# Performance work log

Measured on AMD Instinct MI355X. Metric: run time of the kernel, lower is better.

Reference implementation:

```python
import jax, jax.numpy as jnp
import numpy as np

# Dims: B=8 episodes, N=5 ways, K=5 shots -> BNK=200; L=128 tokens; D=O=1024; R=50 dep relations.
BNK, L, D, O, R = 200, 128, 1024, 1024, 50
M = BNK * L  # flattened token count


def setup_inputs() -> dict:
    key = jax.random.key(0)
    ks = jax.random.split(key, 12)
    rep = jax.random.normal(ks[0], (BNK, L, D), dtype=jnp.float32)
    # edge list: (source sentence in [0,BNK), source token in [0,L))
    arc_sent = jax.random.randint(ks[1], (M, 1), 0, BNK, dtype=jnp.int32)
    arc_tok = jax.random.randint(ks[2], (M, 1), 0, L, dtype=jnp.int32)
    adj_arc_in = jnp.concatenate([arc_sent, arc_tok], axis=1)
    adj_lab_in = jax.random.randint(ks[3], (M,), 0, R, dtype=jnp.int32)
    adj_mask_in = (jax.random.uniform(ks[4], (M, 1)) < 0.9).astype(jnp.float32)
    adj_mask_loop = jnp.ones((M, 1), dtype=jnp.float32)
    mask = (jax.random.uniform(ks[5], (BNK, L)) < 0.9).astype(jnp.float32)
    xav = (2.0 / (D + O)) ** 0.5  # xavier_normal std
    W_in = jax.random.normal(ks[6], (D, O), dtype=jnp.float32) * xav
    b_in = jnp.zeros((R, O), dtype=jnp.float32)
    W_gate_in = jax.random.uniform(ks[7], (D, 1), dtype=jnp.float32)
    b_gate_in = jnp.ones((R, 1), dtype=jnp.float32)
    W_self = jax.random.normal(ks[8], (D, O), dtype=jnp.float32) * xav
    W_gate_self = jax.random.uniform(ks[9], (D, 1), dtype=jnp.float32)
    return {
        "rep": rep, "adj_arc_in": adj_arc_in, "adj_lab_in": adj_lab_in,
        "adj_mask_in": adj_mask_in, "adj_mask_loop": adj_mask_loop, "mask": mask,
        "W_in": W_in, "b_in": b_in, "W_gate_in": W_gate_in, "b_gate_in": b_gate_in,
        "W_self": W_self, "W_gate_self": W_gate_self,
    }


def reference(rep, adj_arc_in, adj_lab_in, adj_mask_in, adj_mask_loop, mask,
              W_in, b_in, W_gate_in, b_gate_in, W_self, W_gate_self):
    bnk, l, d = rep.shape
    o = W_in.shape[1]
    rep_ = rep.reshape(bnk * l, d)                          # (M, D)
    idx = adj_arc_in[:, 0] * l + adj_arc_in[:, 1]           # (M,) flat gather index
    # in-arc potentials: gather projected source token + relation bias
    in_ = (rep_ @ W_in)[idx] + b_in[adj_lab_in]             # (M, O)
    in_gate = (rep_ @ W_gate_in)[idx] + b_gate_in[adj_lab_in]  # (M, 1)
    # self-loop potentials
    same_ = rep_ @ W_self                                   # (M, O)
    same_gate = rep_ @ W_gate_self                          # (M, 1)
    pot = jnp.stack([in_, same_], axis=1)                   # (M, deg=2, O)
    gates = jnp.concatenate([in_gate, same_gate], axis=1)   # (M, 2)
    mask_soft = jnp.concatenate([adj_mask_in, adj_mask_loop], axis=1)  # (M, 2)
    # faithful to original: potentials * mask_soft * (sigmoid(gate) * mask_soft)
    w = mask_soft * (jax.nn.sigmoid(gates) * mask_soft)     # (M, 2)
    out = jax.nn.relu(jnp.einsum('mdo,md->mo', pot, w))     # (M, O)
    return out.reshape(bnk, l, o) * mask[:, :, None]
```

## Files before the change

### kernel.cpp

```cpp
#include <hip/hip_runtime.h>

constexpr int BNKv = 200, Lv = 128, Dv = 1024, Ov = 1024;
constexpr int Mv = BNKv * Lv;
constexpr int KA = 1024;
constexpr int NB = 2048;
constexpr int NT = KA / 64;

using u16 = unsigned short;
typedef __bf16 bf16x8 __attribute__((ext_vector_type(8)));
typedef float f32x4 __attribute__((ext_vector_type(4)));

__device__ __forceinline__ u16 f2bf(float x) {
    unsigned int u = __float_as_uint(x);
    u += 0x7fffu + ((u >> 16) & 1u);
    return (u16)(u >> 16);
}

#define MEMBAR() asm volatile("" ::: "memory")
__device__ __forceinline__ void sbar() {
    MEMBAR(); __builtin_amdgcn_s_barrier(); MEMBAR();
}


__global__ __launch_bounds__(256) void convert_rep(
    const float* __restrict__ rep,
    const float* __restrict__ wg_in,
    const float* __restrict__ wg_self,
    u16* __restrict__ Ap,
    float* __restrict__ gout_in,
    float* __restrict__ gout_self)
{
    const int m = blockIdx.x;
    const int t = threadIdx.x;
    const float4 x  = *(const float4*)(rep + (size_t)m * Dv + t * 4);
    const float4 wi = *(const float4*)(wg_in + t * 4);
    const float4 wsf= *(const float4*)(wg_self + t * 4);

    ushort4 hv = make_ushort4(f2bf(x.x), f2bf(x.y), f2bf(x.z), f2bf(x.w));
    const int cs = (t * 4) ^ ((m & 7) << 3);
    *(ushort4*)(Ap + (size_t)m * KA + cs) = hv;

    float gi = x.x * wi.x + x.y * wi.y + x.z * wi.z + x.w * wi.w;
    float gs = x.x * wsf.x + x.y * wsf.y + x.z * wsf.z + x.w * wsf.w;
#pragma unroll
    for (int off = 32; off > 0; off >>= 1) {
        gi += __shfl_down(gi, off);
        gs += __shfl_down(gs, off);
    }
    __shared__ float ri[4], rs[4];
    if ((t & 63) == 0) { ri[t >> 6] = gi; rs[t >> 6] = gs; }
    __syncthreads();
    if (t == 0) {
        gout_in[m]   = ri[0] + ri[1] + ri[2] + ri[3];
        gout_self[m] = rs[0] + rs[1] + rs[2] + rs[3];
    }
}

__global__ __launch_bounds__(256) void convert_w(
    const float* __restrict__ W0, const float* __restrict__ W1,
    u16* __restrict__ Bt)
{
    const float* W = blockIdx.z ? W1 : W0;
    u16* B = Bt + (size_t)blockIdx.z * 1024 * KA;
    const int kt = blockIdx.x, nt = blockIdx.y;
    __shared__ float tile[64][65];
    const int tid = threadIdx.x;
    const int c = tid & 63, r4 = tid >> 6;
#pragma unroll 4
    for (int it = 0; it < 16; ++it) {
        int kl = it * 4 + r4;
        tile[kl][c] = W[(size_t)(kt * 64 + kl) * Ov + nt * 64 + c];
    }
    __syncthreads();
#pragma unroll 4
    for (int it = 0; it < 16; ++it) {
        int nl = it * 4 + r4;
        const int n = nt * 64 + nl;
        const int kx = kt * 64 + (c ^ ((n & 7) << 3));
        B[(size_t)n * KA + kx] = f2bf(tile[c][nl]);
    }
}

__global__ __launch_bounds__(512) void gemm8p(
    const u16* __restrict__ A, const u16* __restrict__ Bt,
    float* __restrict__ P)
{
    __shared__ u16 As[2][2][128][64];
    __shared__ u16 Bs[2][2][128][64];

    const int tid = threadIdx.x;
    const int l = tid & 63;
    const int w = tid >> 6;
    const int wr = w >> 2;
    const int wc = w & 3;
    const int hc = wc >> 1;
    const int mt = blockIdx.x >> 3;
    const int nt = blockIdx.x & 7;
    const int gm0 = mt * 256, gn0 = nt * 256;
    const int lrow = l & 15;
    const int lk = (l >> 4) * 8;
    const int swz = (lrow & 7) << 3;
    const int c0 = lk ^ swz, c1 = (32 + lk) ^ swz;
    const int srow = w * 8 + (l >> 3);
    const int scol = (l & 7) * 8;

    auto stageA = [&](int kt, int h, int b) {
        const int kb = kt * 64;
#pragma unroll
        for (int r = 0; r < 2; ++r) {
            const u16* g = A + (size_t)(gm0 + h * 128 + r * 64 + srow) * KA + kb + scol;
            __builtin_amdgcn_global_load_lds(
                (const __attribute__((address_space(1))) void*)g,
                (__attribute__((address_space(3))) void*)(&As[b][h][r * 64 + w * 8][0]),
                16, 0, 0);
        }
    };
    auto stageB = [&](int kt, int h, int b) {
        const int kb = kt * 64;
#pragma unroll
        for (int r = 0; r < 2; ++r) {
            const u16* g = Bt + (size_t)(gn0 + h * 128 + r * 64 + srow) * KA + kb + scol;
            __builtin_amdgcn_global_load_lds(
                (const __attribute__((address_space(1))) void*)g,
                (__attribute__((address_space(3))) void*)(&Bs[b][h][r * 64 + w * 8][0]),
                16, 0, 0);
        }
    };

    f32x4 acc[8][4];
#pragma unroll
    for (int i = 0; i < 8; ++i)
#pragma unroll
        for (int j = 0; j < 4; ++j) acc[i][j] = (f32x4){0.f, 0.f, 0.f, 0.f};

    stageA(0, 0, 0); stageA(0, 1, 0); stageB(0, 0, 0); stageB(0, 1, 0);
    stageA(1, 0, 1); stageA(1, 1, 1); stageB(1, 0, 1); stageB(1, 1, 1);
    asm volatile("s_waitcnt vmcnt(8)" ::: "memory");
    sbar();

    bf16x8 aR[4][2];
    bf16x8 bQ[2][2][2];

    for (int kt = 0; kt < NT; ++kt) {
        const int cur = kt & 1;
        const bool st2 = (kt + 2 < NT);

#pragma unroll
        for (int mi = 0; mi < 4; ++mi) {
            aR[mi][0] = *(const bf16x8*)&As[cur][wr][mi * 16 + lrow][c0];
            aR[mi][1] = *(const bf16x8*)&As[cur][wr][mi * 16 + lrow][c1];
        }
#pragma unroll
        for (int nj = 0; nj < 2; ++nj) {
            bQ[0][nj][0] = *(const bf16x8*)&Bs[cur][hc][(wc & 1) * 64 + nj * 16 + lrow][c0];
            bQ[0][nj][1] = *(const bf16x8*)&Bs[cur][hc][(wc & 1) * 64 + nj * 16 + lrow][c1];
        }
        __builtin_amdgcn_s_setprio(1);
#pragma unroll
        for (int mi = 0; mi < 4; ++mi)
#pragma unroll
            for (int nj = 0; nj < 2; ++nj)
#pragma unroll
                for (int ks = 0; ks < 2; ++ks)
                    acc[mi][nj] = __builtin_amdgcn_mfma_f32_16x16x32_bf16(
                        aR[mi][ks], bQ[0][nj][ks], acc[mi][nj], 0, 0, 0);
        __builtin_amdgcn_s_setprio(0);
        sbar();

#pragma unroll
        for (int nj = 0; nj < 2; ++nj) {
            bQ[1][nj][0] = *(const bf16x8*)&Bs[cur][hc][(wc & 1) * 64 + 32 + nj * 16 + lrow][c0];
            bQ[1][nj][1] = *(const bf16x8*)&Bs[cur][hc][(wc & 1) * 64 + 32 + nj * 16 + lrow][c1];
        }
        __builtin_amdgcn_s_setprio(1);
#pragma unroll
        for (int mi = 0; mi < 4; ++mi)
#pragma unroll
            for (int nj = 0; nj < 2; ++nj)
#pragma unroll
                for (int ks = 0; ks < 2; ++ks)
                    acc[mi][2 + nj] = __builtin_amdgcn_mfma_f32_16x16x32_bf16(
                        aR[mi][ks], bQ[1][nj][ks], acc[mi][2 + nj], 0, 0, 0);
        __builtin_amdgcn_s_setprio(0);
        sbar();

#pragma unroll
        for (int mi = 0; mi < 4; ++mi) {
            aR[mi][0] = *(const bf16x8*)&As[cur][wr][64 + mi * 16 + lrow][c0];
            aR[mi][1] = *(const bf16x8*)&As[cur][wr][64 + mi * 16 + lrow][c1];
        }
        if (st2) { stageB(kt + 2, 0, cur); stageB(kt + 2, 1, cur); }
        __builtin_amdgcn_s_setprio(1);
#pragma unroll
        for (int mi = 0; mi < 4; ++mi)
#pragma unroll
            for (int nj = 0; nj < 2; ++nj)
#pragma unroll
                for (int ks = 0; ks < 2; ++ks)
                    acc[4 + mi][nj] = __builtin_amdgcn_mfma_f32_16x16x32_bf16(
                        aR[mi][ks], bQ[0][nj][ks], acc[4 + mi][nj], 0, 0, 0);
        __builtin_amdgcn_s_setprio(0);
        sbar();

        if (st2) { stageA(kt + 2, 0, cur); stageA(kt + 2, 1, cur); }
        __builtin_amdgcn_s_setprio(1);
#pragma unroll
        for (int mi = 0; mi < 4; ++mi)
#pragma unroll
            for (int nj = 0; nj < 2; ++nj)
#pragma unroll
                for (int ks = 0; ks < 2; ++ks)
                    acc[4 + mi][2 + nj] = __builtin_amdgcn_mfma_f32_16x16x32_bf16(
                        aR[mi][ks], bQ[1][nj][ks], acc[4 + mi][2 + nj], 0, 0, 0);
        __builtin_amdgcn_s_setprio(0);
        if (st2) { asm volatile("s_waitcnt vmcnt(8)" ::: "memory"); }
        else     { asm volatile("s_waitcnt vmcnt(0)" ::: "memory"); }
        sbar();
    }

    const int orow = (l >> 4) * 4, ocol = l & 15;
#pragma unroll
    for (int mi = 0; mi < 8; ++mi)
#pragma unroll
        for (int nj = 0; nj < 4; ++nj) {
            const int col = gn0 + wc * 64 + nj * 16 + ocol;
#pragma unroll
            for (int r = 0; r < 4; ++r) {
                const int row = gm0 + wr * 128 + mi * 16 + orow + r;
                P[(size_t)row * NB + col] = acc[mi][nj][r];
            }
        }
}

__global__ __launch_bounds__(256) void epilogue(
    const float* __restrict__ P,
    const float* __restrict__ g_in, const float* __restrict__ g_self,
    const int* __restrict__ arc, const int* __restrict__ lab,
    const float* __restrict__ am_in, const float* __restrict__ am_loop,
    const float* __restrict__ maskBL,
    const float* __restrict__ b_in, const float* __restrict__ b_gate_in,
    float* __restrict__ out)
{
    const int m = blockIdx.x;
    const int t = threadIdx.x;
    __shared__ float sw0, sw1;
    __shared__ int sgidx, slab;
    if (t == 0) {
        const int gidx = arc[2 * m] * Lv + arc[2 * m + 1];
        const int lb = lab[m];
        const float am = am_in[m], lp = am_loop[m], mk = maskBL[m];
        const float gi = g_in[gidx] + b_gate_in[lb];
        const float gs = g_self[m];
        sw0 = am * am * (1.f / (1.f + expf(-gi))) * mk;
        sw1 = lp * lp * (1.f / (1.f + expf(-gs))) * mk;
        sgidx = gidx;
        slab = lb;
    }
    __syncthreads();
    const float w0 = sw0, w1 = sw1;
    const int c = t * 4;
    const float4 pin = *(const float4*)(P + (size_t)sgidx * NB + c);
    const float4 bi  = *(const float4*)(b_in + (size_t)slab * Ov + c);
    const float4 ps  = *(const float4*)(P + (size_t)m * NB + 1024 + c);
    float4 o;
    o.x = fmaxf(w0 * (pin.x + bi.x) + w1 * ps.x, 0.f);
    o.y = fmaxf(w0 * (pin.y + bi.y) + w1 * ps.y, 0.f);
    o.z = fmaxf(w0 * (pin.z + bi.z) + w1 * ps.z, 0.f);
    o.w = fmaxf(w0 * (pin.w + bi.w) + w1 * ps.w, 0.f);
    *(float4*)(out + (size_t)m * Ov + c) = o;
}

constexpr size_t SZ_A  = (size_t)Mv * KA * 2;
constexpr size_t SZ_B  = (size_t)NB * KA * 2;
constexpr size_t OFF_A  = 0;
constexpr size_t OFF_B  = OFF_A + SZ_A;
constexpr size_t OFF_GI = OFF_B + SZ_B;
constexpr size_t OFF_GS = OFF_GI + (size_t)Mv * 4;
constexpr size_t OFF_P  = OFF_GS + (size_t)Mv * 4;

extern "C" void kernel_launch(void* const* d_in, const int* in_sizes, int n_in,
                              void* d_out, int out_size, void* d_ws, size_t ws_size,
                              hipStream_t stream) {
    const float* rep       = (const float*)d_in[0];
    const int*   arc       = (const int*)d_in[1];
    const int*   lab       = (const int*)d_in[2];
    const float* am_in     = (const float*)d_in[3];
    const float* am_loop   = (const float*)d_in[4];
    const float* maskBL    = (const float*)d_in[5];
    const float* W_in      = (const float*)d_in[6];
    const float* b_in      = (const float*)d_in[7];
    const float* W_gate_in = (const float*)d_in[8];
    const float* b_gate_in = (const float*)d_in[9];
    const float* W_self    = (const float*)d_in[10];
    const float* W_gate_self = (const float*)d_in[11];
    float* out = (float*)d_out;
    char* ws = (char*)d_ws;

    u16*   Ap  = (u16*)(ws + OFF_A);
    u16*   Bt  = (u16*)(ws + OFF_B);
    float* gIn = (float*)(ws + OFF_GI);
    float* gSf = (float*)(ws + OFF_GS);
    float* P   = (float*)(ws + OFF_P);

    convert_rep<<<Mv, 256, 0, stream>>>(rep, W_gate_in, W_gate_self, Ap, gIn, gSf);
    convert_w<<<dim3(16, 16, 2), 256, 0, stream>>>(W_in, W_self, Bt);

    const int gemm_grid = (Mv / 256) * (NB / 256);
    gemm8p<<<gemm_grid, 512, 0, stream>>>(Ap, Bt, P);

    epilogue<<<Mv, 256, 0, stream>>>(P, gIn, gSf, arc, lab, am_in, am_loop,
                                     maskBL, b_in, b_gate_in, out);
}
```

Baseline: 396.1 us.

## Split GEMM into two launches and fuse gather epilogue into self-loop GEMM

The single 2048-wide GEMM is split into two launches. The first computes rep@W_in into a 1024-wide buffer. The second computes rep@W_self and applies the gate, gather, bias, ReLU and mask epilogue directly from the accumulators, which drops the separate epilogue kernel and the write and read-back of the self-loop half of P. convert_rep is also reworked so each wave handles one row, with four rows per block, removing the shared-memory reduction and barrier. The cost is two serialized GEMM launches, and the fused epilogue does scattered per-row gathers from Pin with scalar loads.

```diff
diff --git a/kernel.cpp b/kernel.cpp
--- a/kernel.cpp
+++ b/kernel.cpp
@@ -3,7 +3,6 @@
 constexpr int BNKv = 200, Lv = 128, Dv = 1024, Ov = 1024;
 constexpr int Mv = BNKv * Lv;
 constexpr int KA = 1024;
-constexpr int NB = 2048;
 constexpr int NT = KA / 64;
 
 using u16 = unsigned short;
@@ -30,30 +29,31 @@
     float* __restrict__ gout_in,
     float* __restrict__ gout_self)
 {
-    const int m = blockIdx.x;
-    const int t = threadIdx.x;
-    const float4 x  = *(const float4*)(rep + (size_t)m * Dv + t * 4);
-    const float4 wi = *(const float4*)(wg_in + t * 4);
-    const float4 wsf= *(const float4*)(wg_self + t * 4);
-
-    ushort4 hv = make_ushort4(f2bf(x.x), f2bf(x.y), f2bf(x.z), f2bf(x.w));
-    const int cs = (t * 4) ^ ((m & 7) << 3);
-    *(ushort4*)(Ap + (size_t)m * KA + cs) = hv;
-
-    float gi = x.x * wi.x + x.y * wi.y + x.z * wi.z + x.w * wi.w;
-    float gs = x.x * wsf.x + x.y * wsf.y + x.z * wsf.z + x.w * wsf.w;
+    const int row = blockIdx.x * 4 + (threadIdx.x >> 6);
+    const int l = threadIdx.x & 63;
+    const float4* rp  = (const float4*)(rep + (size_t)row * Dv);
+    const float4* wip = (const float4*)wg_in;
+    const float4* wsp = (const float4*)wg_self;
+    u16* ap = Ap + (size_t)row * KA;
+    const int sw = (row & 7) << 3;
+    float gi = 0.f, gs = 0.f;
+#pragma unroll
+    for (int j = 0; j < 4; ++j) {
+        const int c4 = j * 64 + l;
+        const float4 x  = rp[c4];
+        const float4 wi = wip[c4];
+        const float4 wf = wsp[c4];
+        ushort4 hv = make_ushort4(f2bf(x.x), f2bf(x.y), f2bf(x.z), f2bf(x.w));
+        *(ushort4*)(ap + ((c4 * 4) ^ sw)) = hv;
+        gi += x.x * wi.x + x.y * wi.y + x.z * wi.z + x.w * wi.w;
+        gs += x.x * wf.x + x.y * wf.y + x.z * wf.z + x.w * wf.w;
+    }
 #pragma unroll
     for (int off = 32; off > 0; off >>= 1) {
         gi += __shfl_down(gi, off);
         gs += __shfl_down(gs, off);
     }
-    __shared__ float ri[4], rs[4];
-    if ((t & 63) == 0) { ri[t >> 6] = gi; rs[t >> 6] = gs; }
-    __syncthreads();
-    if (t == 0) {
-        gout_in[m]   = ri[0] + ri[1] + ri[2] + ri[3];
-        gout_self[m] = rs[0] + rs[1] + rs[2] + rs[3];
-    }
+    if (l == 0) { gout_in[row] = gi; gout_self[row] = gs; }
 }
 
 __global__ __launch_bounds__(256) void convert_w(
@@ -81,12 +81,21 @@
     }
 }
 
+template <bool FUSED>
 __global__ __launch_bounds__(512) void gemm8p(
     const u16* __restrict__ A, const u16* __restrict__ Bt,
-    float* __restrict__ P)
+    float* __restrict__ OutP,
+    const float* __restrict__ Pin,
+    const float* __restrict__ g_in, const float* __restrict__ g_self,
+    const int* __restrict__ arc, const int* __restrict__ lab,
+    const float* __restrict__ am_in, const float* __restrict__ am_loop,
+    const float* __restrict__ maskBL,
+    const float* __restrict__ b_in, const float* __restrict__ b_gate_in)
 {
     __shared__ u16 As[2][2][128][64];
     __shared__ u16 Bs[2][2][128][64];
+    __shared__ float w0s[FUSED ? 256 : 1], w1s[FUSED ? 256 : 1];
+    __shared__ int  pidx[FUSED ? 256 : 1], plab[FUSED ? 256 : 1];
 
     const int tid = threadIdx.x;
     const int l = tid & 63;
@@ -94,8 +103,8 @@
     const int wr = w >> 2;
     const int wc = w & 3;
     const int hc = wc >> 1;
-    const int mt = blockIdx.x >> 3;
-    const int nt = blockIdx.x & 7;
+    const int mt = blockIdx.x >> 2;
+    const int nt = blockIdx.x & 3;
     const int gm0 = mt * 256, gn0 = nt * 256;
     const int lrow = l & 15;
     const int lk = (l >> 4) * 8;
@@ -104,6 +113,21 @@
     const int srow = w * 8 + (l >> 3);
     const int scol = (l & 7) * 8;
 
+    if constexpr (FUSED) {
+        if (tid < 256) {
+            const int m = gm0 + tid;
+            const int gidx = arc[2 * m] * Lv + arc[2 * m + 1];
+            const int lb = lab[m];
+            const float am = am_in[m], lp = am_loop[m], mk = maskBL[m];
+            const float gi = g_in[gidx] + b_gate_in[lb];
+            const float gs = g_self[m];
+            w0s[tid] = am * am * (1.f / (1.f + expf(-gi))) * mk;
+            w1s[tid] = lp * lp * (1.f / (1.f + expf(-gs))) * mk;
+            pidx[tid] = gidx;
+            plab[tid] = lb;
+        }
+    }
+
     auto stageA = [&](int kt, int h, int b) {
         const int kb = kt * 64;
 #pragma unroll
@@ -219,59 +243,42 @@
     }
 
     const int orow = (l >> 4) * 4, ocol = l & 15;
-#pragma unroll
-    for (int mi = 0; mi < 8; ++mi)
-#pragma unroll
-        for (int nj = 0; nj < 4; ++nj) {
-            const int col = gn0 + wc * 64 + nj * 16 + ocol;
+    if constexpr (!FUSED) {
+#pragma unroll
+        for (int mi = 0; mi < 8; ++mi)
+#pragma unroll
+            for (int nj = 0; nj < 4; ++nj) {
+                const int col = gn0 + wc * 64 + nj * 16 + ocol;
+#pragma unroll
+                for (int r = 0; r < 4; ++r) {
+                    const int row = gm0 + wr * 128 + mi * 16 + orow + r;
+                    OutP[(size_t)row * Ov + col] = acc[mi][nj][r];
+                }
+            }
+    } else {
+#pragma unroll
+        for (int mi = 0; mi < 8; ++mi) {
 #pragma unroll
             for (int r = 0; r < 4; ++r) {
-                const int row = gm0 + wr * 128 + mi * 16 + orow + r;
-                P[(size_t)row * NB + col] = acc[mi][nj][r];
+                const int rloc = wr * 128 + mi * 16 + orow + r;
+                const float w0 = w0s[rloc], w1 = w1s[rloc];
+                const size_t prow = (size_t)pidx[rloc] * Ov;
+                const size_t brow = (size_t)plab[rloc] * Ov;
+                const size_t grow = (size_t)(gm0 + rloc) * Ov;
+#pragma unroll
+                for (int nj = 0; nj < 4; ++nj) {
+                    const int col = gn0 + wc * 64 + nj * 16 + ocol;
+                    const float pin = Pin[prow + col] + b_in[brow + col];
+                    const float v = w0 * pin + w1 * acc[mi][nj][r];
+                    OutP[grow + col] = fmaxf(v, 0.f);
+                }
             }
         }
-}
-
-__global__ __launch_bounds__(256) void epilogue(
-    const float* __restrict__ P,
-    const float* __restrict__ g_in, const float* __restrict__ g_self,
-    const int* __restrict__ arc, const int* __restrict__ lab,
-    const float* __restrict__ am_in, const float* __restrict__ am_loop,
-    const float* __restrict__ maskBL,
-    const float* __restrict__ b_in, const float* __restrict__ b_gate_in,
-    float* __restrict__ out)
-{
-    const int m = blockIdx.x;
-    const int t = threadIdx.x;
-    __shared__ float sw0, sw1;
-    __shared__ int sgidx, slab;
-    if (t == 0) {
-        const int gidx = arc[2 * m] * Lv + arc[2 * m + 1];
-        const int lb = lab[m];
-        const float am = am_in[m], lp = am_loop[m], mk = maskBL[m];
-        const float gi = g_in[gidx] + b_gate_in[lb];
-        const float gs = g_self[m];
-        sw0 = am * am * (1.f / (1.f + expf(-gi))) * mk;
-        sw1 = lp * lp * (1.f / (1.f + expf(-gs))) * mk;
-        sgidx = gidx;
-        slab = lb;
-    }
-    __syncthreads();
-    const float w0 = sw0, w1 = sw1;
-    const int c = t * 4;
-    const float4 pin = *(const float4*)(P + (size_t)sgidx * NB + c);
-    const float4 bi  = *(const float4*)(b_in + (size_t)slab * Ov + c);
-    const float4 ps  = *(const float4*)(P + (size_t)m * NB + 1024 + c);
-    float4 o;
-    o.x = fmaxf(w0 * (pin.x + bi.x) + w1 * ps.x, 0.f);
-    o.y = fmaxf(w0 * (pin.y + bi.y) + w1 * ps.y, 0.f);
-    o.z = fmaxf(w0 * (pin.z + bi.z) + w1 * ps.z, 0.f);
-    o.w = fmaxf(w0 * (pin.w + bi.w) + w1 * ps.w, 0.f);
-    *(float4*)(out + (size_t)m * Ov + c) = o;
+    }
 }
 
 constexpr size_t SZ_A  = (size_t)Mv * KA * 2;
-constexpr size_t SZ_B  = (size_t)NB * KA * 2;
+constexpr size_t SZ_B  = (size_t)2 * 1024 * KA * 2;
 constexpr size_t OFF_A  = 0;
 constexpr size_t OFF_B  = OFF_A + SZ_A;
 constexpr size_t OFF_GI = OFF_B + SZ_B;
@@ -298,16 +305,19 @@
 
     u16*   Ap  = (u16*)(ws + OFF_A);
     u16*   Bt  = (u16*)(ws + OFF_B);
+    u16*   BtS = Bt + (size_t)1024 * KA;
     float* gIn = (float*)(ws + OFF_GI);
     float* gSf = (float*)(ws + OFF_GS);
-    float* P   = (float*)(ws + OFF_P);
-
-    convert_rep<<<Mv, 256, 0, stream>>>(rep, W_gate_in, W_gate_self, Ap, gIn, gSf);
+    float* Pin = (float*)(ws + OFF_P);
+
+    convert_rep<<<Mv / 4, 256, 0, stream>>>(rep, W_gate_in, W_gate_self, Ap, gIn, gSf);
     convert_w<<<dim3(16, 16, 2), 256, 0, stream>>>(W_in, W_self, Bt);
 
-    const int gemm_grid = (Mv / 256) * (NB / 256);
-    gemm8p<<<gemm_grid, 512, 0, stream>>>(Ap, Bt, P);
-
-    epilogue<<<Mv, 256, 0, stream>>>(P, gIn, gSf, arc, lab, am_in, am_loop,
-                                     maskBL, b_in, b_gate_in, out);
-}
+    const int grid = (Mv / 256) * (1024 / 256);
+    gemm8p<false><<<grid, 512, 0, stream>>>(
+        Ap, Bt, Pin, nullptr, nullptr, nullptr, nullptr, nullptr,
+        nullptr, nullptr, nullptr, nullptr, nullptr);
+    gemm8p<true><<<grid, 512, 0, stream>>>(
+        Ap, BtS, out, Pin, gIn, gSf, arc, lab, am_in, am_loop,
+        maskBL, b_in, b_gate_in);
+}
```

Measured after the change: 362.1 us. 1.09x faster.
